# Performance work log

Hardware: AMD Instinct MI355X
Metric: run time of the kernel (lower is better)

The kernel has to match this reference:

```python
import jax, jax.numpy as jnp
import numpy as np

B, N, M, C = 256, 2048, 64, 512
OUT = 3 * M + 6  # fc_write output: [M,1,1,3,1,M,M]


def setup_inputs() -> dict:
    key = jax.random.key(0)
    k0, k1, k2, k3, k4 = jax.random.split(key, 5)
    xavier = 1.4 * np.sqrt(6.0 / (C + OUT))  # xavier_uniform gain=1.4 scale
    return {
        "h": jax.random.normal(k0, (B, C), jnp.float32),
        "w_prev": jax.nn.softmax(jax.random.normal(k1, (B, N), jnp.float32), axis=1),
        "memory": jax.random.normal(k2, (B, N, M), jnp.float32),
        "W": jax.random.uniform(k3, (OUT, C), jnp.float32, -xavier, xavier),
        "b": 0.01 * jax.random.normal(k4, (OUT,), jnp.float32),
    }


def reference(h, w_prev, memory, W, b):
    # controller projection + split
    o = h @ W.T + b  # [B, 3M+6]
    bounds = np.cumsum([M, 1, 1, 3, 1, M])
    k, beta, g, s, gamma, e, a = jnp.split(o, bounds, axis=1)
    beta = jax.nn.softplus(beta)            # [B,1]
    g = jax.nn.sigmoid(g)                   # [B,1]
    s = jax.nn.softmax(s, axis=1)           # [B,3] shift weights {-1,0,+1}
    gamma = 1.0 + jax.nn.softplus(gamma)    # [B,1]
    e = jax.nn.sigmoid(e)                   # [B,M]

    # content addressing: cosine similarity + softmax
    mem_e = memory + 1e-16
    k_e = k + 1e-16
    sim = jnp.einsum('bnm,bm->bn', mem_e, k_e)
    denom = jnp.maximum(
        jnp.linalg.norm(mem_e, axis=-1) * jnp.linalg.norm(k_e, axis=-1, keepdims=True),
        1e-8,
    )
    w_c = jax.nn.softmax(beta * sim / denom, axis=1)  # [B,N]

    # interpolation gate
    w_g = g * w_c + (1.0 - g) * w_prev

    # circular shift convolution (3 taps)
    w_t = (jnp.roll(w_g, 1, axis=1) * s[:, 0:1]
           + w_g * s[:, 1:2]
           + jnp.roll(w_g, -1, axis=1) * s[:, 2:3])

    # sharpening
    w_s = w_t ** gamma
    w = w_s / (jnp.sum(w_s, axis=1, keepdims=True) + 1e-16)  # [B,N]

    # erase/add memory write
    erase = jnp.einsum('bn,bm->bnm', w, e)
    add = jnp.einsum('bn,bm->bnm', w, a)
    mem_new = memory * (1.0 - erase) + add
    return w, mem_new
```

## Files before the change

### kernel.cpp

```cpp
#include <hip/hip_runtime.h>
#include <stdint.h>

#define BB   256
#define NN   2048
#define MM   64
#define CC   512
#define OUTD 198

#define OS_STRIDE 200
#define OS_OFF    0
#define LG_OFF    (BB * OS_STRIDE)
#define MXP_OFF   (LG_OFF + BB * NN)
#define SEP_OFF   (MXP_OFF + BB * 8)
#define PTP_OFF   (SEP_OFF + BB * 8)

typedef float vf4 __attribute__((ext_vector_type(4)));

__device__ __forceinline__ float softplusf(float x) {
    return x > 20.f ? x : log1pf(expf(x));
}
__device__ __forceinline__ float sigmoidf(float x) {
    return 1.f / (1.f + expf(-x));
}

__device__ __forceinline__ float bred_max(float v, float* red) {
    #pragma unroll
    for (int off = 32; off; off >>= 1) v = fmaxf(v, __shfl_down(v, off, 64));
    if ((threadIdx.x & 63) == 0) red[threadIdx.x >> 6] = v;
    __syncthreads();
    float r = fmaxf(fmaxf(red[0], red[1]), fmaxf(red[2], red[3]));
    __syncthreads();
    return r;
}
__device__ __forceinline__ float bred_sum(float v, float* red) {
    #pragma unroll
    for (int off = 32; off; off >>= 1) v += __shfl_down(v, off, 64);
    if ((threadIdx.x & 63) == 0) red[threadIdx.x >> 6] = v;
    __syncthreads();
    float r = red[0] + red[1] + red[2] + red[3];
    __syncthreads();
    return r;
}

__global__ __launch_bounds__(256, 8) void k_ctrl(
        const float* __restrict__ h, const float* __restrict__ Wm,
        const float* __restrict__ bias, float* __restrict__ ws) {
    __shared__ float hs[CC];
    const int b = blockIdx.x >> 3, c = blockIdx.x & 7, t = threadIdx.x;
    hs[t]       = h[(size_t)b * CC + t];
    hs[t + 256] = h[(size_t)b * CC + t + 256];
    __syncthreads();

    const int slot = t >> 3, l8 = t & 7;
    const int r = c * 25 + slot;
    if (slot < 25 && r < OUTD) {
        const float* wr = Wm + (size_t)r * CC + l8 * 64;
        const float* hp = hs + l8 * 64;
        float acc = 0.f;
        #pragma unroll
        for (int q = 0; q < 16; ++q) {
            const float4 p = *(const float4*)(wr + q * 4);
            acc += p.x * hp[q*4+0] + p.y * hp[q*4+1] + p.z * hp[q*4+2] + p.w * hp[q*4+3];
        }
        acc += __shfl_xor(acc, 1, 64);
        acc += __shfl_xor(acc, 2, 64);
        acc += __shfl_xor(acc, 4, 64);
        if (l8 == 0) ws[OS_OFF + b * OS_STRIDE + r] = acc + bias[r];
    }
}

__global__ __launch_bounds__(256, 8) void k_logits(
        const float* __restrict__ mem, float* __restrict__ ws) {
    __shared__ __align__(16) float kk[MM];
    __shared__ float sc[2];
    __shared__ float lgl[256];
    __shared__ float red[4];
    const int b = blockIdx.x >> 3, c = blockIdx.x & 7, t = threadIdx.x;
    const float* osb = ws + OS_OFF + (size_t)b * OS_STRIDE;

    if (t < 64) {
        const float kv = osb[t] + 1e-16f;
        kk[t] = kv;
        float ss = kv * kv;
        #pragma unroll
        for (int off = 32; off; off >>= 1) ss += __shfl_xor(ss, off, 64);
        if (t == 0) sc[0] = sqrtf(ss);
    } else if (t == 64) {
        sc[1] = softplusf(osb[64]);
    }
    __syncthreads();

    const int l = t & 15, grp = t >> 4;
    float kv0 = kk[4*l+0], kv1 = kk[4*l+1], kv2 = kk[4*l+2], kv3 = kk[4*l+3];
    const float beta = sc[1], knorm = sc[0];
    const int row0 = c * 256;
    #pragma unroll
    for (int it = 0; it < 16; ++it) {
        const int row = row0 + it * 16 + grp;
        const float4 p = *(const float4*)(mem + ((size_t)b * NN + row) * MM + 4 * l);
        const float m0 = p.x + 1e-16f, m1 = p.y + 1e-16f;
        const float m2 = p.z + 1e-16f, m3 = p.w + 1e-16f;
        float dot = m0 * kv0 + m1 * kv1 + m2 * kv2 + m3 * kv3;
        float ss  = m0 * m0 + m1 * m1 + m2 * m2 + m3 * m3;
        #pragma unroll
        for (int off = 1; off < 16; off <<= 1) {
            dot += __shfl_xor(dot, off, 64);
            ss  += __shfl_xor(ss,  off, 64);
        }
        if (l == 0) {
            const float lgv = beta * dot / fmaxf(sqrtf(ss) * knorm, 1e-8f);
            ws[LG_OFF + (size_t)b * NN + row] = lgv;
            lgl[it * 16 + grp] = lgv;
        }
    }
    __syncthreads();

    const float v  = lgl[t];
    const float mx = bred_max(v, red);
    const float se = bred_sum(expf(v - mx), red);
    if (t == 0) {
        ws[MXP_OFF + b * 8 + c] = mx;
        ws[SEP_OFF + b * 8 + c] = se;
    }
}

__global__ __launch_bounds__(256, 8) void k_sharp(
        const float* __restrict__ w_prev, float* __restrict__ ws,
        float* __restrict__ w_out) {
    __shared__ float wgc[258];
    __shared__ float sc[7];
    __shared__ float red[4];
    const int b = blockIdx.x >> 3, c = blockIdx.x & 7, t = threadIdx.x;
    const float* osb = ws + OS_OFF + (size_t)b * OS_STRIDE;

    if (t == 0) {
        sc[0] = sigmoidf(osb[65]);
        sc[1] = 1.f + softplusf(osb[69]);
        const float x0 = osb[66], x1 = osb[67], x2 = osb[68];
        const float m3 = fmaxf(x0, fmaxf(x1, x2));
        const float e0 = expf(x0 - m3), e1 = expf(x1 - m3), e2 = expf(x2 - m3);
        const float i3 = 1.f / (e0 + e1 + e2);
        sc[2] = e0 * i3; sc[3] = e1 * i3; sc[4] = e2 * i3;
        float mx = -1e30f;
        #pragma unroll
        for (int j = 0; j < 8; ++j) mx = fmaxf(mx, ws[MXP_OFF + b * 8 + j]);
        float tot = 0.f;
        #pragma unroll
        for (int j = 0; j < 8; ++j)
            tot += ws[SEP_OFF + b * 8 + j] * expf(ws[MXP_OFF + b * 8 + j] - mx);
        sc[5] = mx; sc[6] = 1.f / tot;
    }
    __syncthreads();
    const float g = sc[0], gamma = sc[1];
    const float s0 = sc[2], s1 = sc[3], s2 = sc[4];
    const float mx = sc[5], invtot = sc[6];

    for (int j = t; j < 258; j += 256) {
        const int r = (c * 256 - 1 + j) & (NN - 1);
        const float wc = expf(ws[LG_OFF + (size_t)b * NN + r] - mx) * invtot;
        wgc[j] = g * wc + (1.f - g) * w_prev[(size_t)b * NN + r];
    }
    __syncthreads();

    const float wt = wgc[t] * s0 + wgc[t + 1] * s1 + wgc[t + 2] * s2;
    const float wsv = (wt > 0.f) ? exp2f(gamma * log2f(wt)) : 0.f;
    w_out[(size_t)b * NN + c * 256 + t] = wsv;
    const float ps = bred_sum(wsv, red);
    if (t == 0) ws[PTP_OFF + b * 8 + c] = ps;
}

__global__ __launch_bounds__(256, 8) void k_write(
        const float* __restrict__ mem, const float* __restrict__ ws,
        float* __restrict__ w_out, float* __restrict__ mem_out) {
    __shared__ float wrow[256];
    __shared__ __align__(16) float ee[MM], aa[MM];
    __shared__ float scp[1];
    const int b = blockIdx.x >> 3, c = blockIdx.x & 7, t = threadIdx.x;
    const float* osb = ws + OS_OFF + (size_t)b * OS_STRIDE;

    if (t == 0) {
        float pt = 0.f;
        #pragma unroll
        for (int j = 0; j < 8; ++j) pt += ws[PTP_OFF + b * 8 + j];
        scp[0] = 1.f / (pt + 1e-16f);
    } else if (t >= 64 && t < 128) {
        ee[t - 64] = sigmoidf(osb[70 + (t - 64)]);
    } else if (t >= 128 && t < 192) {
        aa[t - 128] = osb[134 + (t - 128)];
    }
    __syncthreads();

    const float wv = w_out[(size_t)b * NN + c * 256 + t] * scp[0];
    wrow[t] = wv;
    w_out[(size_t)b * NN + c * 256 + t] = wv;
    __syncthreads();

    const int seg = t & 15, rs = t >> 4;
    const vf4 ev = *(const vf4*)&ee[4 * seg];
    const vf4 av = *(const vf4*)&aa[4 * seg];
    const float* mb = mem + ((size_t)b * NN + c * 256) * MM + 4 * seg;
    float* ob = mem_out + ((size_t)b * NN + c * 256) * MM + 4 * seg;
    #pragma unroll 4
    for (int it = 0; it < 16; ++it) {
        const int rr = it * 16 + rs;
        const float w = wrow[rr];
        const float4 p = *(const float4*)(mb + (size_t)rr * MM);
        vf4 o;
        o.x = p.x * (1.f - w * ev.x) + w * av.x;
        o.y = p.y * (1.f - w * ev.y) + w * av.y;
        o.z = p.z * (1.f - w * ev.z) + w * av.z;
        o.w = p.w * (1.f - w * ev.w) + w * av.w;
        __builtin_nontemporal_store(o, (vf4*)(ob + (size_t)rr * MM));
    }
}

extern "C" void kernel_launch(void* const* d_in, const int* in_sizes, int n_in,
                              void* d_out, int out_size, void* d_ws, size_t ws_size,
                              hipStream_t stream) {
    const float* h      = (const float*)d_in[0];
    const float* w_prev = (const float*)d_in[1];
    const float* memory = (const float*)d_in[2];
    const float* W      = (const float*)d_in[3];
    const float* bias   = (const float*)d_in[4];
    float* out = (float*)d_out;
    float* ws  = (float*)d_ws;

    float* w_out   = out;
    float* mem_out = out + (size_t)BB * NN;

    k_ctrl  <<<BB * 8, 256, 0, stream>>>(h, W, bias, ws);
    k_logits<<<BB * 8, 256, 0, stream>>>(memory, ws);
    k_sharp <<<BB * 8, 256, 0, stream>>>(w_prev, ws, w_out);
    k_write <<<BB * 8, 256, 0, stream>>>(memory, ws, w_out, mem_out);
}
```

Before: 285.4 us.

## Fuse pipeline into cooperative persistent kernel with grid syncs and max-free softmax

Replaces the four separate launches with one cooperative persistent kernel. It runs three phases separated by grid-wide syncs, and keeps a three-kernel fallback for when cooperative launch is unavailable. The softmax drops the running max and subtracts beta, which bounds the cosine logit, so partials become simple sums of exponentials. The sharpening and normalisation are merged into the write phase: each block recomputes the whole 2048-wide sharpened row to get the normaliser locally. This removes one kernel and one global round trip of the logits/weights, at the cost of 8x redundant sharpen work per batch row and grid-sync overhead.

```diff
diff --git a/kernel.cpp b/kernel.cpp
--- a/kernel.cpp
+++ b/kernel.cpp
@@ -1,18 +1,20 @@
 #include <hip/hip_runtime.h>
+#include <hip/hip_cooperative_groups.h>
 #include <stdint.h>
+
+namespace cg = cooperative_groups;
 
 #define BB   256
 #define NN   2048
 #define MM   64
 #define CC   512
 #define OUTD 198
+#define NUNITS (BB * 8)
 
 #define OS_STRIDE 200
 #define OS_OFF    0
-#define LG_OFF    (BB * OS_STRIDE)
-#define MXP_OFF   (LG_OFF + BB * NN)
-#define SEP_OFF   (MXP_OFF + BB * 8)
-#define PTP_OFF   (SEP_OFF + BB * 8)
+#define P_OFF     (BB * OS_STRIDE)
+#define SP_OFF    (P_OFF + BB * NN)
 
 typedef float vf4 __attribute__((ext_vector_type(4)));
 
@@ -23,39 +25,28 @@
     return 1.f / (1.f + expf(-x));
 }
 
-__device__ __forceinline__ float bred_max(float v, float* red) {
+__device__ __forceinline__ float bredsum(float v, float* red) {
     #pragma unroll
-    for (int off = 32; off; off >>= 1) v = fmaxf(v, __shfl_down(v, off, 64));
+    for (int o = 32; o; o >>= 1) v += __shfl_down(v, o, 64);
     if ((threadIdx.x & 63) == 0) red[threadIdx.x >> 6] = v;
     __syncthreads();
-    float r = fmaxf(fmaxf(red[0], red[1]), fmaxf(red[2], red[3]));
+    float r = red[0] + red[1] + red[2] + red[3];
     __syncthreads();
     return r;
 }
-__device__ __forceinline__ float bred_sum(float v, float* red) {
-    #pragma unroll
-    for (int off = 32; off; off >>= 1) v += __shfl_down(v, off, 64);
-    if ((threadIdx.x & 63) == 0) red[threadIdx.x >> 6] = v;
-    __syncthreads();
-    float r = red[0] + red[1] + red[2] + red[3];
-    __syncthreads();
-    return r;
-}
-
-__global__ __launch_bounds__(256, 8) void k_ctrl(
-        const float* __restrict__ h, const float* __restrict__ Wm,
-        const float* __restrict__ bias, float* __restrict__ ws) {
-    __shared__ float hs[CC];
-    const int b = blockIdx.x >> 3, c = blockIdx.x & 7, t = threadIdx.x;
-    hs[t]       = h[(size_t)b * CC + t];
-    hs[t + 256] = h[(size_t)b * CC + t + 256];
-    __syncthreads();
-
-    const int slot = t >> 3, l8 = t & 7;
-    const int r = c * 25 + slot;
+
+__device__ __forceinline__ void phaseA(int u, const float* __restrict__ h,
+        const float* __restrict__ Wm, const float* __restrict__ bias,
+        float* __restrict__ ws, float* sm) {
+    const int b = u >> 3, c = u & 7, t = threadIdx.x;
+    __syncthreads();
+    sm[t]       = h[(size_t)b * CC + t];
+    sm[t + 256] = h[(size_t)b * CC + t + 256];
+    __syncthreads();
+    const int slot = t >> 3, l8 = t & 7, r = c * 25 + slot;
     if (slot < 25 && r < OUTD) {
         const float* wr = Wm + (size_t)r * CC + l8 * 64;
-        const float* hp = hs + l8 * 64;
+        const float* hp = sm + l8 * 64;
         float acc = 0.f;
         #pragma unroll
         for (int q = 0; q < 16; ++q) {
@@ -69,130 +60,107 @@
     }
 }
 
-__global__ __launch_bounds__(256, 8) void k_logits(
-        const float* __restrict__ mem, float* __restrict__ ws) {
-    __shared__ __align__(16) float kk[MM];
-    __shared__ float sc[2];
-    __shared__ float lgl[256];
-    __shared__ float red[4];
-    const int b = blockIdx.x >> 3, c = blockIdx.x & 7, t = threadIdx.x;
+__device__ __forceinline__ void phaseB(int u, const float* __restrict__ mem,
+        float* __restrict__ ws, float* sm) {
+    const int b = u >> 3, c = u & 7, t = threadIdx.x;
+    float* kk = sm;
+    float* sc = sm + 64;
+    float* red = sm + 72;
     const float* osb = ws + OS_OFF + (size_t)b * OS_STRIDE;
-
+    __syncthreads();
     if (t < 64) {
         const float kv = osb[t] + 1e-16f;
         kk[t] = kv;
-        float ss = kv * kv;
-        #pragma unroll
-        for (int off = 32; off; off >>= 1) ss += __shfl_xor(ss, off, 64);
-        if (t == 0) sc[0] = sqrtf(ss);
+        float ssq = kv * kv;
+        #pragma unroll
+        for (int o = 32; o; o >>= 1) ssq += __shfl_xor(ssq, o, 64);
+        if (t == 0) sc[0] = sqrtf(ssq);
     } else if (t == 64) {
         sc[1] = softplusf(osb[64]);
     }
     __syncthreads();
-
     const int l = t & 15, grp = t >> 4;
-    float kv0 = kk[4*l+0], kv1 = kk[4*l+1], kv2 = kk[4*l+2], kv3 = kk[4*l+3];
-    const float beta = sc[1], knorm = sc[0];
-    const int row0 = c * 256;
-    #pragma unroll
+    const float kv0 = kk[4*l], kv1 = kk[4*l+1], kv2 = kk[4*l+2], kv3 = kk[4*l+3];
+    const float knorm = sc[0], beta = sc[1];
+    float psum = 0.f;
+    #pragma unroll 4
     for (int it = 0; it < 16; ++it) {
-        const int row = row0 + it * 16 + grp;
+        const int row = c * 256 + it * 16 + grp;
         const float4 p = *(const float4*)(mem + ((size_t)b * NN + row) * MM + 4 * l);
         const float m0 = p.x + 1e-16f, m1 = p.y + 1e-16f;
         const float m2 = p.z + 1e-16f, m3 = p.w + 1e-16f;
         float dot = m0 * kv0 + m1 * kv1 + m2 * kv2 + m3 * kv3;
-        float ss  = m0 * m0 + m1 * m1 + m2 * m2 + m3 * m3;
-        #pragma unroll
-        for (int off = 1; off < 16; off <<= 1) {
-            dot += __shfl_xor(dot, off, 64);
-            ss  += __shfl_xor(ss,  off, 64);
+        float ssq = m0 * m0 + m1 * m1 + m2 * m2 + m3 * m3;
+        #pragma unroll
+        for (int o = 1; o < 16; o <<= 1) {
+            dot += __shfl_xor(dot, o, 64);
+            ssq += __shfl_xor(ssq, o, 64);
         }
         if (l == 0) {
-            const float lgv = beta * dot / fmaxf(sqrtf(ss) * knorm, 1e-8f);
-            ws[LG_OFF + (size_t)b * NN + row] = lgv;
-            lgl[it * 16 + grp] = lgv;
-        }
-    }
-    __syncthreads();
-
-    const float v  = lgl[t];
-    const float mx = bred_max(v, red);
-    const float se = bred_sum(expf(v - mx), red);
+            const float lg = beta * dot / fmaxf(sqrtf(ssq) * knorm, 1e-8f);
+            const float pv = expf(lg - beta);
+            ws[P_OFF + (size_t)b * NN + row] = pv;
+            psum += pv;
+        }
+    }
+    const float tot = bredsum(psum, red);
+    if (t == 0) ws[SP_OFF + b * 8 + c] = tot;
+}
+
+__device__ __forceinline__ void phaseC(int u, const float* __restrict__ w_prev,
+        const float* __restrict__ mem, float* __restrict__ ws,
+        float* __restrict__ w_out, float* __restrict__ mem_out, float* sm) {
+    const int b = u >> 3, c = u & 7, t = threadIdx.x;
+    float* wg  = sm;
+    float* sc  = sm + 2050;
+    float* ee  = sm + 2064;
+    float* aa  = sm + 2128;
+    float* red = sm + 2192;
+    const float* osb = ws + OS_OFF + (size_t)b * OS_STRIDE;
+    __syncthreads();
     if (t == 0) {
-        ws[MXP_OFF + b * 8 + c] = mx;
-        ws[SEP_OFF + b * 8 + c] = se;
-    }
-}
-
-__global__ __launch_bounds__(256, 8) void k_sharp(
-        const float* __restrict__ w_prev, float* __restrict__ ws,
-        float* __restrict__ w_out) {
-    __shared__ float wgc[258];
-    __shared__ float sc[7];
-    __shared__ float red[4];
-    const int b = blockIdx.x >> 3, c = blockIdx.x & 7, t = threadIdx.x;
-    const float* osb = ws + OS_OFF + (size_t)b * OS_STRIDE;
-
-    if (t == 0) {
+        float S1 = 0.f;
+        #pragma unroll
+        for (int j = 0; j < 8; ++j) S1 += ws[SP_OFF + b * 8 + j];
+        sc[5] = 1.f / S1;
         sc[0] = sigmoidf(osb[65]);
         sc[1] = 1.f + softplusf(osb[69]);
         const float x0 = osb[66], x1 = osb[67], x2 = osb[68];
-        const float m3 = fmaxf(x0, fmaxf(x1, x2));
-        const float e0 = expf(x0 - m3), e1 = expf(x1 - m3), e2 = expf(x2 - m3);
-        const float i3 = 1.f / (e0 + e1 + e2);
-        sc[2] = e0 * i3; sc[3] = e1 * i3; sc[4] = e2 * i3;
-        float mx = -1e30f;
-        #pragma unroll
-        for (int j = 0; j < 8; ++j) mx = fmaxf(mx, ws[MXP_OFF + b * 8 + j]);
-        float tot = 0.f;
-        #pragma unroll
-        for (int j = 0; j < 8; ++j)
-            tot += ws[SEP_OFF + b * 8 + j] * expf(ws[MXP_OFF + b * 8 + j] - mx);
-        sc[5] = mx; sc[6] = 1.f / tot;
-    }
-    __syncthreads();
-    const float g = sc[0], gamma = sc[1];
-    const float s0 = sc[2], s1 = sc[3], s2 = sc[4];
-    const float mx = sc[5], invtot = sc[6];
-
-    for (int j = t; j < 258; j += 256) {
-        const int r = (c * 256 - 1 + j) & (NN - 1);
-        const float wc = expf(ws[LG_OFF + (size_t)b * NN + r] - mx) * invtot;
-        wgc[j] = g * wc + (1.f - g) * w_prev[(size_t)b * NN + r];
-    }
-    __syncthreads();
-
-    const float wt = wgc[t] * s0 + wgc[t + 1] * s1 + wgc[t + 2] * s2;
-    const float wsv = (wt > 0.f) ? exp2f(gamma * log2f(wt)) : 0.f;
-    w_out[(size_t)b * NN + c * 256 + t] = wsv;
-    const float ps = bred_sum(wsv, red);
-    if (t == 0) ws[PTP_OFF + b * 8 + c] = ps;
-}
-
-__global__ __launch_bounds__(256, 8) void k_write(
-        const float* __restrict__ mem, const float* __restrict__ ws,
-        float* __restrict__ w_out, float* __restrict__ mem_out) {
-    __shared__ float wrow[256];
-    __shared__ __align__(16) float ee[MM], aa[MM];
-    __shared__ float scp[1];
-    const int b = blockIdx.x >> 3, c = blockIdx.x & 7, t = threadIdx.x;
-    const float* osb = ws + OS_OFF + (size_t)b * OS_STRIDE;
-
-    if (t == 0) {
-        float pt = 0.f;
-        #pragma unroll
-        for (int j = 0; j < 8; ++j) pt += ws[PTP_OFF + b * 8 + j];
-        scp[0] = 1.f / (pt + 1e-16f);
+        const float mx = fmaxf(x0, fmaxf(x1, x2));
+        const float e0 = expf(x0 - mx), e1 = expf(x1 - mx), e2 = expf(x2 - mx);
+        const float iv = 1.f / (e0 + e1 + e2);
+        sc[2] = e0 * iv; sc[3] = e1 * iv; sc[4] = e2 * iv;
     } else if (t >= 64 && t < 128) {
         ee[t - 64] = sigmoidf(osb[70 + (t - 64)]);
     } else if (t >= 128 && t < 192) {
         aa[t - 128] = osb[134 + (t - 128)];
     }
     __syncthreads();
-
-    const float wv = w_out[(size_t)b * NN + c * 256 + t] * scp[0];
-    wrow[t] = wv;
-    w_out[(size_t)b * NN + c * 256 + t] = wv;
+    const float g = sc[0], gamma = sc[1];
+    const float s0 = sc[2], s1 = sc[3], s2 = sc[4], inv1 = sc[5];
+
+    for (int j = t; j < 2050; j += 256) {
+        const int r = (j + NN - 1) & (NN - 1);
+        const float wc = ws[P_OFF + (size_t)b * NN + r] * inv1;
+        wg[j] = g * wc + (1.f - g) * w_prev[(size_t)b * NN + r];
+    }
+    __syncthreads();
+
+    float myw = 0.f, pp = 0.f;
+    #pragma unroll
+    for (int i = 0; i < 8; ++i) {
+        const int n = t + i * 256;
+        const float wt = wg[n] * s0 + wg[n + 1] * s1 + wg[n + 2] * s2;
+        const float wsv = (wt > 0.f) ? exp2f(gamma * log2f(wt)) : 0.f;
+        pp += wsv;
+        if (i == c) myw = wsv;
+    }
+    const float ptot = bredsum(pp, red);
+    const float invp = 1.f / (ptot + 1e-16f);
+    const float wfin = myw * invp;
+    w_out[(size_t)b * NN + c * 256 + t] = wfin;
+    __syncthreads();
+    wg[t] = wfin;
     __syncthreads();
 
     const int seg = t & 15, rs = t >> 4;
@@ -203,7 +171,7 @@
     #pragma unroll 4
     for (int it = 0; it < 16; ++it) {
         const int rr = it * 16 + rs;
-        const float w = wrow[rr];
+        const float w = wg[rr];
         const float4 p = *(const float4*)(mb + (size_t)rr * MM);
         vf4 o;
         o.x = p.x * (1.f - w * ev.x) + w * av.x;
@@ -212,6 +180,43 @@
         o.w = p.w * (1.f - w * ev.w) + w * av.w;
         __builtin_nontemporal_store(o, (vf4*)(ob + (size_t)rr * MM));
     }
+}
+
+__global__ __launch_bounds__(256, 8) void k_coop(
+        const float* __restrict__ h, const float* __restrict__ w_prev,
+        const float* __restrict__ mem, const float* __restrict__ Wm,
+        const float* __restrict__ bias, float* __restrict__ ws,
+        float* __restrict__ w_out, float* __restrict__ mem_out) {
+    cg::grid_group grid = cg::this_grid();
+    __shared__ __align__(16) float sm[2208];
+    for (int u = blockIdx.x; u < NUNITS; u += gridDim.x) phaseA(u, h, Wm, bias, ws, sm);
+    __threadfence();
+    grid.sync();
+    __threadfence();
+    for (int u = blockIdx.x; u < NUNITS; u += gridDim.x) phaseB(u, mem, ws, sm);
+    __threadfence();
+    grid.sync();
+    __threadfence();
+    for (int u = blockIdx.x; u < NUNITS; u += gridDim.x) phaseC(u, w_prev, mem, ws, w_out, mem_out, sm);
+}
+
+__global__ __launch_bounds__(256, 8) void kA(
+        const float* __restrict__ h, const float* __restrict__ Wm,
+        const float* __restrict__ bias, float* __restrict__ ws) {
+    __shared__ __align__(16) float sm[2208];
+    for (int u = blockIdx.x; u < NUNITS; u += gridDim.x) phaseA(u, h, Wm, bias, ws, sm);
+}
+__global__ __launch_bounds__(256, 8) void kB(
+        const float* __restrict__ mem, float* __restrict__ ws) {
+    __shared__ __align__(16) float sm[2208];
+    for (int u = blockIdx.x; u < NUNITS; u += gridDim.x) phaseB(u, mem, ws, sm);
+}
+__global__ __launch_bounds__(256, 8) void kC(
+        const float* __restrict__ w_prev, const float* __restrict__ mem,
+        float* __restrict__ ws, float* __restrict__ w_out,
+        float* __restrict__ mem_out) {
+    __shared__ __align__(16) float sm[2208];
+    for (int u = blockIdx.x; u < NUNITS; u += gridDim.x) phaseC(u, w_prev, mem, ws, w_out, mem_out, sm);
 }
 
 extern "C" void kernel_launch(void* const* d_in, const int* in_sizes, int n_in,
@@ -228,8 +233,36 @@
     float* w_out   = out;
     float* mem_out = out + (size_t)BB * NN;
 
-    k_ctrl  <<<BB * 8, 256, 0, stream>>>(h, W, bias, ws);
-    k_logits<<<BB * 8, 256, 0, stream>>>(memory, ws);
-    k_sharp <<<BB * 8, 256, 0, stream>>>(w_prev, ws, w_out);
-    k_write <<<BB * 8, 256, 0, stream>>>(memory, ws, w_out, mem_out);
-}
+    static int gridB = -1;
+    static int useCoop = 1;
+    if (gridB < 0) {
+        int dev = 0;
+        (void)hipGetDevice(&dev);
+        hipDeviceProp_t prop;
+        (void)hipGetDeviceProperties(&prop, dev);
+        int maxB = 0;
+        if (hipOccupancyMaxActiveBlocksPerMultiprocessor(&maxB, (const void*)k_coop, 256, 0)
+                != hipSuccess || maxB < 1) maxB = 1;
+        long cap = (long)maxB * (long)prop.multiProcessorCount;
+        gridB = (int)(cap < NUNITS ? cap : NUNITS);
+        if (gridB < 1) gridB = 256;
+        int coopAttr = 0;
+        (void)hipDeviceGetAttribute(&coopAttr, hipDeviceAttributeCooperativeLaunch, dev);
+        if (!coopAttr) useCoop = 0;
+    }
+
+    if (useCoop) {
+        void* args[] = {(void*)&h, (void*)&w_prev, (void*)&memory, (void*)&W,
+                        (void*)&bias, (void*)&ws, (void*)&w_out, (void*)&mem_out};
+        if (hipLaunchCooperativeKernel((const void*)k_coop, dim3(gridB), dim3(256),
+                                       args, 0, stream) != hipSuccess) {
+            useCoop = 0;
+            (void)hipGetLastError();
+        }
+    }
+    if (!useCoop) {
+        kA<<<NUNITS, 256, 0, stream>>>(h, W, bias, ws);
+        kB<<<NUNITS, 256, 0, stream>>>(memory, ws);
+        kC<<<NUNITS, 256, 0, stream>>>(w_prev, memory, ws, w_out, mem_out);
+    }
+}
```

Result: slower. 821.1 us (+187.7%).
